# Kernel optimization log

Hardware: AMD Instinct MI355X
Metric: run time of the kernel (lower is better)

The kernel has to match this reference:

```python
import jax, jax.numpy as jnp
import numpy as np

N = 100000
E = 1600000
IN_FEATS = 512
HIDDEN = 128
NUM_CLASSES = 2


def setup_inputs() -> dict:
    key = jax.random.key(0)
    k1, k2, k3, k4, k5, k6, k7 = jax.random.split(key, 7)
    inputs = jax.random.normal(k1, (N, IN_FEATS), dtype=jnp.float32)
    src = jax.random.randint(k2, (E,), 0, N, dtype=jnp.int64)
    dst = jax.random.randint(k3, (E,), 0, N, dtype=jnp.int64)
    # Glorot-style init like DGL GraphConv
    s1 = (6.0 / (IN_FEATS + HIDDEN)) ** 0.5
    s2 = (6.0 / (HIDDEN + NUM_CLASSES)) ** 0.5
    W1 = jax.random.uniform(k4, (IN_FEATS, HIDDEN), jnp.float32, -s1, s1)
    b1 = jnp.zeros((HIDDEN,), jnp.float32)
    W2 = jax.random.uniform(k5, (HIDDEN, NUM_CLASSES), jnp.float32, -s2, s2)
    b2 = jnp.zeros((NUM_CLASSES,), jnp.float32)
    return {"inputs": inputs, "W1": W1, "b1": b1, "W2": W2, "b2": b2,
            "src": src, "dst": dst}


def _graph_conv(x, W, b, src, dst, norm_src, norm_dst):
    # DGL GraphConv, norm='both': D_dst^{-1/2} A D_src^{-1/2} X W + b
    xw = x @ W                                   # [N, out] dense GEMM first (in >= out)
    m = (xw * norm_src[:, None])[src]            # gather messages [E, out]
    agg = jax.ops.segment_sum(m, dst, num_segments=N)  # scatter-add [N, out]
    return agg * norm_dst[:, None] + b


def reference(inputs, W1, b1, W2, b2, src, dst):
    ones = jnp.ones((src.shape[0],), jnp.float32)
    out_deg = jax.ops.segment_sum(ones, src, num_segments=N)
    in_deg = jax.ops.segment_sum(ones, dst, num_segments=N)
    norm_src = jax.lax.rsqrt(jnp.maximum(out_deg, 1.0))
    norm_dst = jax.lax.rsqrt(jnp.maximum(in_deg, 1.0))

    h = _graph_conv(inputs, W1, b1, src, dst, norm_src, norm_dst)
    h = jax.nn.relu(h)
    # dropout is identity at inference (training=False)
    h = _graph_conv(h, W2, b2, src, dst, norm_src, norm_dst)
    return jax.nn.softmax(h, axis=1)
```

## Files before the change

kernel.cpp:

```cpp
#include <hip/hip_runtime.h>
#include <math.h>

#define N_NODES 100000
#define N_EDGES 1600000
#define IN_F    512
#define HID     128

#define SH      8
#define NPB     256
#define BINS    ((N_NODES + NPB - 1) / NPB)
#define CBLK    256
#define EPB     ((N_EDGES + CBLK - 1) / CBLK)

typedef __attribute__((ext_vector_type(8))) _Float16 half8;
typedef __attribute__((ext_vector_type(2))) _Float16 half2v;
typedef __attribute__((ext_vector_type(4))) float float4v;

__global__ __launch_bounds__(256) void hist_kernel(const int* __restrict__ src,
                                                   const int* __restrict__ dst,
                                                   int* __restrict__ dbh, int* __restrict__ sbh) {
    __shared__ int hd[BINS], hs[BINS];
    const int t = threadIdx.x, blk = blockIdx.x;
    for (int i = t; i < BINS; i += 256) { hd[i] = 0; hs[i] = 0; }
    __syncthreads();
    const int e0 = blk * EPB, e1 = min(N_EDGES, e0 + EPB);
    for (int e = e0 + t; e < e1; e += 256) {
        atomicAdd(&hd[dst[e] >> SH], 1);
        atomicAdd(&hs[src[e] >> SH], 1);
    }
    __syncthreads();
    for (int i = t; i < BINS; i += 256) {
        dbh[i * CBLK + blk] = hd[i];
        sbh[i * CBLK + blk] = hs[i];
    }
}

__global__ __launch_bounds__(256) void binscan_kernel(int* __restrict__ dbh, int* __restrict__ sbh,
                                                      int* __restrict__ dtot, int* __restrict__ stot) {
    __shared__ int sh[256];
    const int b = blockIdx.x, t = threadIdx.x;
    int* arr; int* tot;
    if (b < BINS) { arr = dbh + (size_t)b * CBLK; tot = &dtot[b]; }
    else          { arr = sbh + (size_t)(b - BINS) * CBLK; tot = &stot[b - BINS]; }
    int v = arr[t];
    sh[t] = v; __syncthreads();
#pragma unroll
    for (int d = 1; d < 256; d <<= 1) {
        int u = (t >= d) ? sh[t - d] : 0;
        __syncthreads();
        sh[t] += u;
        __syncthreads();
    }
    arr[t] = sh[t] - v;
    if (t == 255) *tot = sh[255];
}

__global__ __launch_bounds__(512) void binbase_kernel(const int* __restrict__ dtot,
                                                      const int* __restrict__ stot,
                                                      int* __restrict__ dbase, int* __restrict__ sbase,
                                                      int* __restrict__ offs) {
    __shared__ int sh[512];
    const int t = threadIdx.x;
    int v = (t < BINS) ? dtot[t] : 0;
    sh[t] = v; __syncthreads();
#pragma unroll
    for (int d = 1; d < 512; d <<= 1) {
        int u = (t >= d) ? sh[t - d] : 0;
        __syncthreads();
        sh[t] += u;
        __syncthreads();
    }
    if (t < BINS) dbase[t] = sh[t] - v;
    if (t == BINS - 1) { dbase[BINS] = sh[t]; offs[N_NODES] = sh[t]; }
    __syncthreads();
    int v2 = (t < BINS) ? stot[t] : 0;
    sh[t] = v2; __syncthreads();
#pragma unroll
    for (int d = 1; d < 512; d <<= 1) {
        int u = (t >= d) ? sh[t - d] : 0;
        __syncthreads();
        sh[t] += u;
        __syncthreads();
    }
    if (t < BINS) sbase[t] = sh[t] - v2;
    if (t == BINS - 1) sbase[BINS] = sh[t];
}

__global__ __launch_bounds__(256) void scatter_bins_kernel(const int* __restrict__ src,
                                                           const int* __restrict__ dst,
                                                           const int* __restrict__ dbh,
                                                           const int* __restrict__ sbh,
                                                           const int* __restrict__ dbase,
                                                           const int* __restrict__ sbase,
                                                           int* __restrict__ ds_dst,
                                                           int* __restrict__ ds_src,
                                                           int* __restrict__ ss_src) {
    __shared__ int dcur[BINS], scur[BINS];
    const int t = threadIdx.x, blk = blockIdx.x;
    for (int i = t; i < BINS; i += 256) {
        dcur[i] = dbase[i] + dbh[i * CBLK + blk];
        scur[i] = sbase[i] + sbh[i * CBLK + blk];
    }
    __syncthreads();
    const int e0 = blk * EPB, e1 = min(N_EDGES, e0 + EPB);
    for (int e = e0 + t; e < e1; e += 256) {
        int d = dst[e], s = src[e];
        int p = atomicAdd(&dcur[d >> SH], 1);
        ds_dst[p] = d; ds_src[p] = s;
        int q = atomicAdd(&scur[s >> SH], 1);
        ss_src[q] = s;
    }
}

__global__ __launch_bounds__(256) void finalize_kernel(const int* __restrict__ ds_dst,
                                                       const int* __restrict__ ds_src,
                                                       const int* __restrict__ ss_src,
                                                       const int* __restrict__ dbase,
                                                       const int* __restrict__ sbase,
                                                       int* __restrict__ csr, int* __restrict__ offs,
                                                       float* __restrict__ norm_dst,
                                                       float* __restrict__ norm_src) {
    __shared__ int cnt[NPB], pos[NPB];
    const int t = threadIdx.x, b = blockIdx.x;
    if (b < BINS) {
        const int start = dbase[b], end = dbase[b + 1];
        cnt[t] = 0; __syncthreads();
        for (int k = start + t; k < end; k += 256)
            atomicAdd(&cnt[ds_dst[k] & (NPB - 1)], 1);
        __syncthreads();
        const int c = cnt[t];
        pos[t] = c; __syncthreads();
#pragma unroll
        for (int d = 1; d < 256; d <<= 1) {
            int u = (t >= d) ? pos[t - d] : 0;
            __syncthreads();
            pos[t] += u;
            __syncthreads();
        }
        const int excl = pos[t] - c;
        const int node = (b << SH) + t;
        if (node < N_NODES) {
            offs[node] = start + excl;
            norm_dst[node] = rsqrtf(fmaxf((float)c, 1.0f));
        }
        cnt[t] = start + excl;
        __syncthreads();
        for (int k = start + t; k < end; k += 256) {
            int dl = ds_dst[k] & (NPB - 1);
            int p = atomicAdd(&cnt[dl], 1);
            csr[p] = ds_src[k];
        }
    } else {
        const int bb = b - BINS;
        const int start = sbase[bb], end = sbase[bb + 1];
        cnt[t] = 0; __syncthreads();
        for (int k = start + t; k < end; k += 256)
            atomicAdd(&cnt[ss_src[k] & (NPB - 1)], 1);
        __syncthreads();
        const int node = (bb << SH) + t;
        if (node < N_NODES)
            norm_src[node] = rsqrtf(fmaxf((float)cnt[t], 1.0f));
    }
}

__global__ void cvtW1_kernel(const float* __restrict__ W1, _Float16* __restrict__ W1T) {
    int i = blockIdx.x * blockDim.x + threadIdx.x;
    if (i < IN_F * HID) {
        int k = i >> 7, c = i & 127;
        W1T[(size_t)c * IN_F + k] = (_Float16)W1[i];
    }
}

#define APAD 40
__global__ __launch_bounds__(256) void gemm1_mfma_kernel(const float* __restrict__ X,
                                                         const _Float16* __restrict__ W1T,
                                                         const float* __restrict__ norm_src,
                                                         _Float16* __restrict__ xwh) {
    __shared__ _Float16 As[2][128 * APAD];

    const int t    = threadIdx.x;
    const int wave = t >> 6;
    const int lane = t & 63;
    const int m0   = blockIdx.x * 128;
    const int quad = lane >> 4;
    const int l16  = lane & 15;

    float4v acc[2][8];
#pragma unroll
    for (int r = 0; r < 2; r++)
#pragma unroll
        for (int c = 0; c < 8; c++) acc[r][c] = (float4v)0.f;

    const int srow = t >> 1;
    const int sc16 = (t & 1) * 16;
    const int sgrow = m0 + srow;
    const bool svalid = sgrow < N_NODES;
    const float* xbase = X + (size_t)sgrow * IN_F + sc16;

    float4 va[4];
#pragma unroll
    for (int i = 0; i < 4; i++) va[i] = make_float4(0.f, 0.f, 0.f, 0.f);
    if (svalid) {
        const float4* xp = reinterpret_cast<const float4*>(xbase);
        va[0] = xp[0]; va[1] = xp[1]; va[2] = xp[2]; va[3] = xp[3];
    }
    half8 bfrag[8];
#pragma unroll
    for (int ct = 0; ct < 8; ct++)
        bfrag[ct] = *reinterpret_cast<const half8*>(&W1T[(size_t)(ct * 16 + l16) * IN_F + quad * 8]);

    {
        half8 h0, h1;
        h0[0]=(_Float16)va[0].x; h0[1]=(_Float16)va[0].y; h0[2]=(_Float16)va[0].z; h0[3]=(_Float16)va[0].w;
        h0[4]=(_Float16)va[1].x; h0[5]=(_Float16)va[1].y; h0[6]=(_Float16)va[1].z; h0[7]=(_Float16)va[1].w;
        h1[0]=(_Float16)va[2].x; h1[1]=(_Float16)va[2].y; h1[2]=(_Float16)va[2].z; h1[3]=(_Float16)va[2].w;
        h1[4]=(_Float16)va[3].x; h1[5]=(_Float16)va[3].y; h1[6]=(_Float16)va[3].z; h1[7]=(_Float16)va[3].w;
        *reinterpret_cast<half8*>(&As[0][srow * APAD + sc16 + 0]) = h0;
        *reinterpret_cast<half8*>(&As[0][srow * APAD + sc16 + 8]) = h1;
    }

    int cur = 0;
    for (int it = 0; it < IN_F / 32; it++) {
        const int ktn = (it + 1) * 32;
        const bool more = ktn < IN_F;
        __syncthreads();

        float4 vb[4];
        half8 bnext[8];
        if (more) {
            if (svalid) {
                const float4* xp = reinterpret_cast<const float4*>(xbase + ktn);
                vb[0] = xp[0]; vb[1] = xp[1]; vb[2] = xp[2]; vb[3] = xp[3];
            } else {
                vb[0] = vb[1] = vb[2] = vb[3] = make_float4(0.f, 0.f, 0.f, 0.f);
            }
#pragma unroll
            for (int ct = 0; ct < 8; ct++)
                bnext[ct] = *reinterpret_cast<const half8*>(
                    &W1T[(size_t)(ct * 16 + l16) * IN_F + ktn + quad * 8]);
        }

        half8 afrag[2];
#pragma unroll
        for (int r = 0; r < 2; r++)
            afrag[r] = *reinterpret_cast<const half8*>(
                &As[cur][(wave * 32 + r * 16 + l16) * APAD + quad * 8]);
#pragma unroll
        for (int r = 0; r < 2; r++)
#pragma unroll
            for (int ct = 0; ct < 8; ct++)
                acc[r][ct] = __builtin_amdgcn_mfma_f32_16x16x32_f16(afrag[r], bfrag[ct], acc[r][ct], 0, 0, 0);

        if (more) {
            half8 h0, h1;
            h0[0]=(_Float16)vb[0].x; h0[1]=(_Float16)vb[0].y; h0[2]=(_Float16)vb[0].z; h0[3]=(_Float16)vb[0].w;
            h0[4]=(_Float16)vb[1].x; h0[5]=(_Float16)vb[1].y; h0[6]=(_Float16)vb[1].z; h0[7]=(_Float16)vb[1].w;
            h1[0]=(_Float16)vb[2].x; h1[1]=(_Float16)vb[2].y; h1[2]=(_Float16)vb[2].z; h1[3]=(_Float16)vb[2].w;
            h1[4]=(_Float16)vb[3].x; h1[5]=(_Float16)vb[3].y; h1[6]=(_Float16)vb[3].z; h1[7]=(_Float16)vb[3].w;
            *reinterpret_cast<half8*>(&As[cur ^ 1][srow * APAD + sc16 + 0]) = h0;
            *reinterpret_cast<half8*>(&As[cur ^ 1][srow * APAD + sc16 + 8]) = h1;
#pragma unroll
            for (int ct = 0; ct < 8; ct++) bfrag[ct] = bnext[ct];
        }
        cur ^= 1;
    }

#pragma unroll
    for (int r = 0; r < 2; r++) {
#pragma unroll
        for (int i = 0; i < 4; i++) {
            int grow = m0 + wave * 32 + r * 16 + quad * 4 + i;
            if (grow < N_NODES) {
                float s = norm_src[grow];
                _Float16* orow = &xwh[(size_t)grow * HID];
#pragma unroll
                for (int ct = 0; ct < 8; ct++)
                    orow[ct * 16 + l16] = (_Float16)(acc[r][ct][i] * s);
            }
        }
    }
}

__global__ __launch_bounds__(256) void gather1_kernel(
        const int* __restrict__ csr, const int* __restrict__ offs,
        const _Float16* __restrict__ xwh, const float* __restrict__ norm_dst,
        const float* __restrict__ norm_src, const float* __restrict__ b1,
        const float* __restrict__ W2, float* __restrict__ hw2) {
    const int w    = (blockIdx.x * blockDim.x + threadIdx.x) >> 6;
    const int lane = threadIdx.x & 63;
    if (w >= N_NODES) return;
    const int off = offs[w], end = offs[w + 1];
    const int j2 = lane * 2;

    float a0 = 0.f, a1 = 0.f;
    int k = off;
    for (; k + 4 <= end; k += 4) {
        int s0 = csr[k], s1 = csr[k + 1], s2 = csr[k + 2], s3 = csr[k + 3];
        half2v v0 = *reinterpret_cast<const half2v*>(&xwh[(size_t)s0 * HID + j2]);
        half2v v1 = *reinterpret_cast<const half2v*>(&xwh[(size_t)s1 * HID + j2]);
        half2v v2 = *reinterpret_cast<const half2v*>(&xwh[(size_t)s2 * HID + j2]);
        half2v v3 = *reinterpret_cast<const half2v*>(&xwh[(size_t)s3 * HID + j2]);
        a0 += (float)v0[0] + (float)v1[0] + (float)v2[0] + (float)v3[0];
        a1 += (float)v0[1] + (float)v1[1] + (float)v2[1] + (float)v3[1];
    }
    for (; k < end; k++) {
        half2v v = *reinterpret_cast<const half2v*>(&xwh[(size_t)csr[k] * HID + j2]);
        a0 += (float)v[0]; a1 += (float)v[1];
    }

    const float nd = norm_dst[w];
    float2 b = *reinterpret_cast<const float2*>(&b1[j2]);
    float h0 = fmaxf(a0 * nd + b.x, 0.f);
    float h1 = fmaxf(a1 * nd + b.y, 0.f);
    float2 w2a = reinterpret_cast<const float2*>(W2)[j2];
    float2 w2b = reinterpret_cast<const float2*>(W2)[j2 + 1];
    float p0 = h0 * w2a.x + h1 * w2b.x;
    float p1 = h0 * w2a.y + h1 * w2b.y;
#pragma unroll
    for (int offd = 32; offd > 0; offd >>= 1) {
        p0 += __shfl_down(p0, offd);
        p1 += __shfl_down(p1, offd);
    }
    if (lane == 0) {
        float ns = norm_src[w];
        reinterpret_cast<float2*>(hw2)[w] = make_float2(p0 * ns, p1 * ns);
    }
}

__global__ void gather2_softmax_kernel(
        const int* __restrict__ csr, const int* __restrict__ offs,
        const float* __restrict__ hw2, const float* __restrict__ norm_dst,
        const float* __restrict__ b2, float* __restrict__ out) {
    const int w    = (blockIdx.x * blockDim.x + threadIdx.x) >> 6;
    const int lane = threadIdx.x & 63;
    const int sub  = lane >> 4, k0 = lane & 15;
    const int n = w * 4 + sub;
    if (n >= N_NODES) return;
    const int off = offs[n], end = offs[n + 1];

    float a0 = 0.f, a1 = 0.f;
    for (int k = off + k0; k < end; k += 16) {
        int s = csr[k];
        float2 v = reinterpret_cast<const float2*>(hw2)[s];
        a0 += v.x; a1 += v.y;
    }
#pragma unroll
    for (int d = 1; d < 16; d <<= 1) {
        a0 += __shfl_xor(a0, d);
        a1 += __shfl_xor(a1, d);
    }
    if (k0 == 0) {
        float nd = norm_dst[n];
        float z0 = a0 * nd + b2[0];
        float z1 = a1 * nd + b2[1];
        float m = fmaxf(z0, z1);
        float e0 = expf(z0 - m), e1 = expf(z1 - m);
        float inv = 1.f / (e0 + e1);
        reinterpret_cast<float2*>(out)[n] = make_float2(e0 * inv, e1 * inv);
    }
}

extern "C" void kernel_launch(void* const* d_in, const int* in_sizes, int n_in,
                              void* d_out, int out_size, void* d_ws, size_t ws_size,
                              hipStream_t stream) {
    const float* X   = (const float*)d_in[0];
    const float* W1  = (const float*)d_in[1];
    const float* b1  = (const float*)d_in[2];
    const float* W2  = (const float*)d_in[3];
    const float* b2  = (const float*)d_in[4];
    const int*   src = (const int*)d_in[5];
    const int*   dst = (const int*)d_in[6];
    float* out = (float*)d_out;

    const size_t N = N_NODES;
    char* ws = (char*)d_ws;
    int*   dbh      = (int*)ws;   ws += (size_t)BINS * CBLK * 4;
    int*   sbh      = (int*)ws;   ws += (size_t)BINS * CBLK * 4;
    int*   dtot     = (int*)ws;   ws += BINS * 4;
    int*   stot     = (int*)ws;   ws += BINS * 4;
    int*   dbase    = (int*)ws;   ws += (BINS + 1) * 4;
    int*   sbase    = (int*)ws;   ws += (BINS + 1) * 4;
    int*   ds_dst   = (int*)ws;   ws += (size_t)N_EDGES * 4;
    int*   ds_src   = (int*)ws;   ws += (size_t)N_EDGES * 4;
    int*   ss_src   = (int*)ws;   ws += (size_t)N_EDGES * 4;
    int*   csr      = (int*)ws;   ws += (size_t)N_EDGES * 4;
    int*   offs     = (int*)ws;   ws += (N + 1) * 4;
    float* norm_src = (float*)ws; ws += N * 4;
    float* norm_dst = (float*)ws; ws += N * 4;
    float* hw2      = (float*)ws; ws += N * 2 * 4;
    _Float16* W1T   = (_Float16*)ws; ws += (size_t)IN_F * HID * 2;
    _Float16* xwh   = (_Float16*)ws; ws += N * (size_t)HID * 2;

    hist_kernel<<<CBLK, 256, 0, stream>>>(src, dst, dbh, sbh);
    binscan_kernel<<<2 * BINS, 256, 0, stream>>>(dbh, sbh, dtot, stot);
    binbase_kernel<<<1, 512, 0, stream>>>(dtot, stot, dbase, sbase, offs);
    scatter_bins_kernel<<<CBLK, 256, 0, stream>>>(src, dst, dbh, sbh, dbase, sbase,
                                                  ds_dst, ds_src, ss_src);
    finalize_kernel<<<2 * BINS, 256, 0, stream>>>(ds_dst, ds_src, ss_src, dbase, sbase,
                                                  csr, offs, norm_dst, norm_src);
    cvtW1_kernel<<<(IN_F * HID + 255) / 256, 256, 0, stream>>>(W1, W1T);
    gemm1_mfma_kernel<<<(N_NODES + 127) / 128, 256, 0, stream>>>(X, W1T, norm_src, xwh);
    gather1_kernel<<<(N_NODES * 64 + 255) / 256, 256, 0, stream>>>(
        csr, offs, xwh, norm_dst, norm_src, b1, W2, hw2);
    gather2_softmax_kernel<<<(((int)N + 3) / 4 * 64 + 255) / 256, 256, 0, stream>>>(
        csr, offs, hw2, norm_dst, b2, out);
}
```

Measured before the change: 524.5 us.

## Replace source-side bin sort with atomic degree count and vectorize layer-1 gather

```diff
diff --git a/kernel.cpp b/kernel.cpp
--- a/kernel.cpp
+++ b/kernel.cpp
@@ -13,35 +13,42 @@
 #define EPB     ((N_EDGES + CBLK - 1) / CBLK)
 
 typedef __attribute__((ext_vector_type(8))) _Float16 half8;
-typedef __attribute__((ext_vector_type(2))) _Float16 half2v;
 typedef __attribute__((ext_vector_type(4))) float float4v;
+
+__global__ __launch_bounds__(256) void prep_kernel(const float* __restrict__ W1,
+                                                   _Float16* __restrict__ W1T,
+                                                   int* __restrict__ sdeg) {
+    int i = blockIdx.x * 256 + threadIdx.x;
+    if (i < IN_F * HID) {
+        int k = i >> 7, c = i & 127;
+        W1T[(size_t)c * IN_F + k] = (_Float16)W1[i];
+    }
+    if (i < N_NODES) sdeg[i] = 0;
+}
 
 __global__ __launch_bounds__(256) void hist_kernel(const int* __restrict__ src,
                                                    const int* __restrict__ dst,
-                                                   int* __restrict__ dbh, int* __restrict__ sbh) {
-    __shared__ int hd[BINS], hs[BINS];
+                                                   int* __restrict__ dbh,
+                                                   int* __restrict__ sdeg) {
+    __shared__ int hd[BINS];
     const int t = threadIdx.x, blk = blockIdx.x;
-    for (int i = t; i < BINS; i += 256) { hd[i] = 0; hs[i] = 0; }
+    for (int i = t; i < BINS; i += 256) hd[i] = 0;
     __syncthreads();
     const int e0 = blk * EPB, e1 = min(N_EDGES, e0 + EPB);
     for (int e = e0 + t; e < e1; e += 256) {
         atomicAdd(&hd[dst[e] >> SH], 1);
-        atomicAdd(&hs[src[e] >> SH], 1);
-    }
-    __syncthreads();
-    for (int i = t; i < BINS; i += 256) {
+        atomicAdd(&sdeg[src[e]], 1);
+    }
+    __syncthreads();
+    for (int i = t; i < BINS; i += 256)
         dbh[i * CBLK + blk] = hd[i];
-        sbh[i * CBLK + blk] = hs[i];
-    }
-}
-
-__global__ __launch_bounds__(256) void binscan_kernel(int* __restrict__ dbh, int* __restrict__ sbh,
-                                                      int* __restrict__ dtot, int* __restrict__ stot) {
+}
+
+__global__ __launch_bounds__(256) void binscan_kernel(int* __restrict__ dbh,
+                                                      int* __restrict__ dtot) {
     __shared__ int sh[256];
     const int b = blockIdx.x, t = threadIdx.x;
-    int* arr; int* tot;
-    if (b < BINS) { arr = dbh + (size_t)b * CBLK; tot = &dtot[b]; }
-    else          { arr = sbh + (size_t)(b - BINS) * CBLK; tot = &stot[b - BINS]; }
+    int* arr = dbh + (size_t)b * CBLK;
     int v = arr[t];
     sh[t] = v; __syncthreads();
 #pragma unroll
@@ -52,12 +59,11 @@
         __syncthreads();
     }
     arr[t] = sh[t] - v;
-    if (t == 255) *tot = sh[255];
+    if (t == 255) dtot[b] = sh[255];
 }
 
 __global__ __launch_bounds__(512) void binbase_kernel(const int* __restrict__ dtot,
-                                                      const int* __restrict__ stot,
-                                                      int* __restrict__ dbase, int* __restrict__ sbase,
+                                                      int* __restrict__ dbase,
                                                       int* __restrict__ offs) {
     __shared__ int sh[512];
     const int t = threadIdx.x;
@@ -72,102 +78,63 @@
     }
     if (t < BINS) dbase[t] = sh[t] - v;
     if (t == BINS - 1) { dbase[BINS] = sh[t]; offs[N_NODES] = sh[t]; }
-    __syncthreads();
-    int v2 = (t < BINS) ? stot[t] : 0;
-    sh[t] = v2; __syncthreads();
-#pragma unroll
-    for (int d = 1; d < 512; d <<= 1) {
-        int u = (t >= d) ? sh[t - d] : 0;
-        __syncthreads();
-        sh[t] += u;
-        __syncthreads();
-    }
-    if (t < BINS) sbase[t] = sh[t] - v2;
-    if (t == BINS - 1) sbase[BINS] = sh[t];
 }
 
 __global__ __launch_bounds__(256) void scatter_bins_kernel(const int* __restrict__ src,
                                                            const int* __restrict__ dst,
                                                            const int* __restrict__ dbh,
-                                                           const int* __restrict__ sbh,
                                                            const int* __restrict__ dbase,
-                                                           const int* __restrict__ sbase,
                                                            int* __restrict__ ds_dst,
-                                                           int* __restrict__ ds_src,
-                                                           int* __restrict__ ss_src) {
-    __shared__ int dcur[BINS], scur[BINS];
+                                                           int* __restrict__ ds_src) {
+    __shared__ int dcur[BINS];
     const int t = threadIdx.x, blk = blockIdx.x;
-    for (int i = t; i < BINS; i += 256) {
+    for (int i = t; i < BINS; i += 256)
         dcur[i] = dbase[i] + dbh[i * CBLK + blk];
-        scur[i] = sbase[i] + sbh[i * CBLK + blk];
-    }
     __syncthreads();
     const int e0 = blk * EPB, e1 = min(N_EDGES, e0 + EPB);
     for (int e = e0 + t; e < e1; e += 256) {
         int d = dst[e], s = src[e];
         int p = atomicAdd(&dcur[d >> SH], 1);
         ds_dst[p] = d; ds_src[p] = s;
-        int q = atomicAdd(&scur[s >> SH], 1);
-        ss_src[q] = s;
     }
 }
 
 __global__ __launch_bounds__(256) void finalize_kernel(const int* __restrict__ ds_dst,
                                                        const int* __restrict__ ds_src,
-                                                       const int* __restrict__ ss_src,
+                                                       const int* __restrict__ sdeg,
                                                        const int* __restrict__ dbase,
-                                                       const int* __restrict__ sbase,
                                                        int* __restrict__ csr, int* __restrict__ offs,
                                                        float* __restrict__ norm_dst,
                                                        float* __restrict__ norm_src) {
     __shared__ int cnt[NPB], pos[NPB];
     const int t = threadIdx.x, b = blockIdx.x;
-    if (b < BINS) {
-        const int start = dbase[b], end = dbase[b + 1];
-        cnt[t] = 0; __syncthreads();
-        for (int k = start + t; k < end; k += 256)
-            atomicAdd(&cnt[ds_dst[k] & (NPB - 1)], 1);
-        __syncthreads();
-        const int c = cnt[t];
-        pos[t] = c; __syncthreads();
-#pragma unroll
-        for (int d = 1; d < 256; d <<= 1) {
-            int u = (t >= d) ? pos[t - d] : 0;
-            __syncthreads();
-            pos[t] += u;
-            __syncthreads();
-        }
-        const int excl = pos[t] - c;
-        const int node = (b << SH) + t;
-        if (node < N_NODES) {
-            offs[node] = start + excl;
-            norm_dst[node] = rsqrtf(fmaxf((float)c, 1.0f));
-        }
-        cnt[t] = start + excl;
-        __syncthreads();
-        for (int k = start + t; k < end; k += 256) {
-            int dl = ds_dst[k] & (NPB - 1);
-            int p = atomicAdd(&cnt[dl], 1);
-            csr[p] = ds_src[k];
-        }
-    } else {
-        const int bb = b - BINS;
-        const int start = sbase[bb], end = sbase[bb + 1];
-        cnt[t] = 0; __syncthreads();
-        for (int k = start + t; k < end; k += 256)
-            atomicAdd(&cnt[ss_src[k] & (NPB - 1)], 1);
-        __syncthreads();
-        const int node = (bb << SH) + t;
-        if (node < N_NODES)
-            norm_src[node] = rsqrtf(fmaxf((float)cnt[t], 1.0f));
-    }
-}
-
-__global__ void cvtW1_kernel(const float* __restrict__ W1, _Float16* __restrict__ W1T) {
-    int i = blockIdx.x * blockDim.x + threadIdx.x;
-    if (i < IN_F * HID) {
-        int k = i >> 7, c = i & 127;
-        W1T[(size_t)c * IN_F + k] = (_Float16)W1[i];
+    const int start = dbase[b], end = dbase[b + 1];
+    cnt[t] = 0; __syncthreads();
+    for (int k = start + t; k < end; k += 256)
+        atomicAdd(&cnt[ds_dst[k] & (NPB - 1)], 1);
+    __syncthreads();
+    const int c = cnt[t];
+    pos[t] = c; __syncthreads();
+#pragma unroll
+    for (int d = 1; d < 256; d <<= 1) {
+        int u = (t >= d) ? pos[t - d] : 0;
+        __syncthreads();
+        pos[t] += u;
+        __syncthreads();
+    }
+    const int excl = pos[t] - c;
+    const int node = (b << SH) + t;
+    if (node < N_NODES) {
+        offs[node] = start + excl;
+        norm_dst[node] = rsqrtf(fmaxf((float)c, 1.0f));
+        norm_src[node] = rsqrtf(fmaxf((float)sdeg[node], 1.0f));
+    }
+    cnt[t] = start + excl;
+    __syncthreads();
+    for (int k = start + t; k < end; k += 256) {
+        int dl = ds_dst[k] & (NPB - 1);
+        int p = atomicAdd(&cnt[dl], 1);
+        csr[p] = ds_src[k];
     }
 }
 
@@ -286,44 +253,63 @@
         const _Float16* __restrict__ xwh, const float* __restrict__ norm_dst,
         const float* __restrict__ norm_src, const float* __restrict__ b1,
         const float* __restrict__ W2, float* __restrict__ hw2) {
-    const int w    = (blockIdx.x * blockDim.x + threadIdx.x) >> 6;
+    const int gw   = (blockIdx.x * blockDim.x + threadIdx.x) >> 6;
     const int lane = threadIdx.x & 63;
-    if (w >= N_NODES) return;
-    const int off = offs[w], end = offs[w + 1];
-    const int j2 = lane * 2;
-
-    float a0 = 0.f, a1 = 0.f;
+    const int sub  = lane >> 4;
+    const int l16  = lane & 15;
+    const int n    = gw * 4 + sub;
+    if (n >= N_NODES) return;
+    const int off = offs[n], end = offs[n + 1];
+    const int j8 = l16 * 8;
+
+    float a[8];
+#pragma unroll
+    for (int i = 0; i < 8; i++) a[i] = 0.f;
+
     int k = off;
     for (; k + 4 <= end; k += 4) {
         int s0 = csr[k], s1 = csr[k + 1], s2 = csr[k + 2], s3 = csr[k + 3];
-        half2v v0 = *reinterpret_cast<const half2v*>(&xwh[(size_t)s0 * HID + j2]);
-        half2v v1 = *reinterpret_cast<const half2v*>(&xwh[(size_t)s1 * HID + j2]);
-        half2v v2 = *reinterpret_cast<const half2v*>(&xwh[(size_t)s2 * HID + j2]);
-        half2v v3 = *reinterpret_cast<const half2v*>(&xwh[(size_t)s3 * HID + j2]);
-        a0 += (float)v0[0] + (float)v1[0] + (float)v2[0] + (float)v3[0];
-        a1 += (float)v0[1] + (float)v1[1] + (float)v2[1] + (float)v3[1];
-    }
-    for (; k < end; k++) {
-        half2v v = *reinterpret_cast<const half2v*>(&xwh[(size_t)csr[k] * HID + j2]);
-        a0 += (float)v[0]; a1 += (float)v[1];
-    }
-
-    const float nd = norm_dst[w];
-    float2 b = *reinterpret_cast<const float2*>(&b1[j2]);
-    float h0 = fmaxf(a0 * nd + b.x, 0.f);
-    float h1 = fmaxf(a1 * nd + b.y, 0.f);
-    float2 w2a = reinterpret_cast<const float2*>(W2)[j2];
-    float2 w2b = reinterpret_cast<const float2*>(W2)[j2 + 1];
-    float p0 = h0 * w2a.x + h1 * w2b.x;
-    float p1 = h0 * w2a.y + h1 * w2b.y;
-#pragma unroll
-    for (int offd = 32; offd > 0; offd >>= 1) {
-        p0 += __shfl_down(p0, offd);
-        p1 += __shfl_down(p1, offd);
-    }
-    if (lane == 0) {
-        float ns = norm_src[w];
-        reinterpret_cast<float2*>(hw2)[w] = make_float2(p0 * ns, p1 * ns);
+        half8 v0 = *reinterpret_cast<const half8*>(&xwh[(size_t)s0 * HID + j8]);
+        half8 v1 = *reinterpret_cast<const half8*>(&xwh[(size_t)s1 * HID + j8]);
+        half8 v2 = *reinterpret_cast<const half8*>(&xwh[(size_t)s2 * HID + j8]);
+        half8 v3 = *reinterpret_cast<const half8*>(&xwh[(size_t)s3 * HID + j8]);
+#pragma unroll
+        for (int i = 0; i < 8; i++)
+            a[i] += ((float)v0[i] + (float)v1[i]) + ((float)v2[i] + (float)v3[i]);
+    }
+    for (; k < end; ++k) {
+        half8 v = *reinterpret_cast<const half8*>(&xwh[(size_t)csr[k] * HID + j8]);
+#pragma unroll
+        for (int i = 0; i < 8; i++) a[i] += (float)v[i];
+    }
+
+    const float nd = norm_dst[n];
+    const float4 b1a = *reinterpret_cast<const float4*>(&b1[j8]);
+    const float4 b1b = *reinterpret_cast<const float4*>(&b1[j8 + 4]);
+    float h[8];
+    h[0] = fmaxf(a[0] * nd + b1a.x, 0.f);
+    h[1] = fmaxf(a[1] * nd + b1a.y, 0.f);
+    h[2] = fmaxf(a[2] * nd + b1a.z, 0.f);
+    h[3] = fmaxf(a[3] * nd + b1a.w, 0.f);
+    h[4] = fmaxf(a[4] * nd + b1b.x, 0.f);
+    h[5] = fmaxf(a[5] * nd + b1b.y, 0.f);
+    h[6] = fmaxf(a[6] * nd + b1b.z, 0.f);
+    h[7] = fmaxf(a[7] * nd + b1b.w, 0.f);
+
+    const float4* w2p = reinterpret_cast<const float4*>(&W2[(size_t)j8 * 2]);
+    float4 q0 = w2p[0], q1 = w2p[1], q2 = w2p[2], q3 = w2p[3];
+    float p0 = h[0]*q0.x + h[1]*q0.z + h[2]*q1.x + h[3]*q1.z
+             + h[4]*q2.x + h[5]*q2.z + h[6]*q3.x + h[7]*q3.z;
+    float p1 = h[0]*q0.y + h[1]*q0.w + h[2]*q1.y + h[3]*q1.w
+             + h[4]*q2.y + h[5]*q2.w + h[6]*q3.y + h[7]*q3.w;
+#pragma unroll
+    for (int d = 1; d < 16; d <<= 1) {
+        p0 += __shfl_xor(p0, d);
+        p1 += __shfl_xor(p1, d);
+    }
+    if (l16 == 0) {
+        float ns = norm_src[n];
+        reinterpret_cast<float2*>(hw2)[n] = make_float2(p0 * ns, p1 * ns);
     }
 }
 
@@ -375,14 +361,11 @@
     const size_t N = N_NODES;
     char* ws = (char*)d_ws;
     int*   dbh      = (int*)ws;   ws += (size_t)BINS * CBLK * 4;
-    int*   sbh      = (int*)ws;   ws += (size_t)BINS * CBLK * 4;
     int*   dtot     = (int*)ws;   ws += BINS * 4;
-    int*   stot     = (int*)ws;   ws += BINS * 4;
     int*   dbase    = (int*)ws;   ws += (BINS + 1) * 4;
-    int*   sbase    = (int*)ws;   ws += (BINS + 1) * 4;
+    int*   sdeg     = (int*)ws;   ws += N * 4;
     int*   ds_dst   = (int*)ws;   ws += (size_t)N_EDGES * 4;
     int*   ds_src   = (int*)ws;   ws += (size_t)N_EDGES * 4;
-    int*   ss_src   = (int*)ws;   ws += (size_t)N_EDGES * 4;
     int*   csr      = (int*)ws;   ws += (size_t)N_EDGES * 4;
     int*   offs     = (int*)ws;   ws += (N + 1) * 4;
     float* norm_src = (float*)ws; ws += N * 4;
@@ -391,16 +374,15 @@
     _Float16* W1T   = (_Float16*)ws; ws += (size_t)IN_F * HID * 2;
     _Float16* xwh   = (_Float16*)ws; ws += N * (size_t)HID * 2;
 
-    hist_kernel<<<CBLK, 256, 0, stream>>>(src, dst, dbh, sbh);
-    binscan_kernel<<<2 * BINS, 256, 0, stream>>>(dbh, sbh, dtot, stot);
-    binbase_kernel<<<1, 512, 0, stream>>>(dtot, stot, dbase, sbase, offs);
-    scatter_bins_kernel<<<CBLK, 256, 0, stream>>>(src, dst, dbh, sbh, dbase, sbase,
-                                                  ds_dst, ds_src, ss_src);
-    finalize_kernel<<<2 * BINS, 256, 0, stream>>>(ds_dst, ds_src, ss_src, dbase, sbase,
-                                                  csr, offs, norm_dst, norm_src);
-    cvtW1_kernel<<<(IN_F * HID + 255) / 256, 256, 0, stream>>>(W1, W1T);
+    prep_kernel<<<(N_NODES + 255) / 256, 256, 0, stream>>>(W1, W1T, sdeg);
+    hist_kernel<<<CBLK, 256, 0, stream>>>(src, dst, dbh, sdeg);
+    binscan_kernel<<<BINS, 256, 0, stream>>>(dbh, dtot);
+    binbase_kernel<<<1, 512, 0, stream>>>(dtot, dbase, offs);
+    scatter_bins_kernel<<<CBLK, 256, 0, stream>>>(src, dst, dbh, dbase, ds_dst, ds_src);
+    finalize_kernel<<<BINS, 256, 0, stream>>>(ds_dst, ds_src, sdeg, dbase,
+                                              csr, offs, norm_dst, norm_src);
     gemm1_mfma_kernel<<<(N_NODES + 127) / 128, 256, 0, stream>>>(X, W1T, norm_src, xwh);
-    gather1_kernel<<<(N_NODES * 64 + 255) / 256, 256, 0, stream>>>(
+    gather1_kernel<<<(((N_NODES + 3) / 4) * 64 + 255) / 256, 256, 0, stream>>>(
         csr, offs, xwh, norm_dst, norm_src, b1, W2, hw2);
     gather2_softmax_kernel<<<(((int)N + 3) / 4 * 64 + 255) / 256, 256, 0, stream>>>(
         csr, offs, hw2, norm_dst, b2, out);
```

Measured after the change: 532.0 us. No clear change (+1.4%).
